# Optimization experiments

Hardware: AMD Instinct MI355X
Metric: run time of the kernel (lower is better)

Reference implementation:

```python
import jax, jax.numpy as jnp
import numpy as np

N = 4_194_304
NUM_ITER = 6
DAMPING = 0.95
TOL = 1e-06
EPS = 1e-12


def _translate_x(dx):
    """4x4 homogeneous translation along the optical (x) axis."""
    return jnp.eye(4, dtype=dx.dtype).at[0, 3].set(dx)


def setup_inputs() -> dict:
    key = jax.random.key(0)
    k1, k2, k3 = jax.random.split(key, 3)
    # Ray origins: near x = -10, transverse spread within/around the aperture
    px = -10.0 + 0.5 * jax.random.normal(k1, (N, 1), dtype=jnp.float32)
    pyz = 8.0 * jax.random.normal(k2, (N, 2), dtype=jnp.float32)
    P = jnp.concatenate([px, pyz], axis=-1)
    # Ray directions: mostly +x, small transverse components, normalized
    vyz = 0.05 * jax.random.normal(k3, (N, 2), dtype=jnp.float32)
    V = jnp.concatenate([jnp.ones((N, 1), jnp.float32), vyz], axis=-1)
    V = V / jnp.linalg.norm(V, axis=-1, keepdims=True)
    tf = jnp.eye(4, dtype=jnp.float32)
    return {
        "P": P,
        "V": V,
        "tf": tf,
        "diameter": jnp.float32(50.0),
        "C": jnp.float32(0.02),
        "anchors": jnp.zeros((2,), jnp.float32),
        "scale": jnp.float32(1.0),
        "normalize": jnp.asarray(False),
    }


def reference(P, V, tf, diameter, C, anchors, scale, normalize):
    # normalize: curvature interpreted relative to semi-diameter
    C_eff = jnp.where(normalize, C * 2.0 / diameter, C)
    s2 = scale * scale

    def sag(r2):  # scaled spherical sag: f = scale * g(r2/scale^2)
        u = r2 / s2
        root = jnp.sqrt(jnp.clip(1.0 - C_eff * C_eff * u, EPS))
        return scale * C_eff * u / (1.0 + root)

    def sag_grad(y, z):  # (df/dy, df/dz) = C*(y,z) / (scale*sqrt(1-C^2 u))
        u = (y * y + z * z) / s2
        root = jnp.sqrt(jnp.clip(1.0 - C_eff * C_eff * u, EPS))
        k = C_eff / (scale * root)
        return k * y, k * z

    # anchors shift the surface along x by fractions of the edge sag (extent)
    extent = sag(jnp.square(diameter * 0.5))
    surface_tf = tf @ _translate_x(-anchors[0] * extent)
    next_tf = tf @ _translate_x((anchors[1] - anchors[0]) * extent)

    # Rays into surface-local frame
    R = surface_tf[:3, :3]
    tv = surface_tf[:3, 3]
    Pl = (P - tv) @ R  # [N,3] = R^T (P - t)
    Vl = V @ R
    vx, vy, vz = Vl[:, 0], Vl[:, 1], Vl[:, 2]

    safe_vx = jnp.where(jnp.abs(vx) > EPS, vx, EPS)
    t = -Pl[:, 0] / safe_vx  # init: intersection with plane x=0

    # Damped Newton on F(t) = sag(y(t),z(t)) - x(t)
    for _ in range(NUM_ITER):
        p = Pl + t[:, None] * Vl
        y, z = p[:, 1], p[:, 2]
        F = sag(y * y + z * z) - p[:, 0]
        gy, gz = sag_grad(y, z)
        dF = gy * vy + gz * vz - vx
        dF = jnp.where(jnp.abs(dF) > EPS, dF, EPS)
        t = t - DAMPING * F / dF

    p = Pl + t[:, None] * Vl
    y, z = p[:, 1], p[:, 2]
    r2 = y * y + z * z
    F = sag(r2) - p[:, 0]
    gy, gz = sag_grad(y, z)
    # implicit-surface normal: grad(sag(y,z) - x) = (-1, gy, gz), normalized
    n_local = jnp.stack([-jnp.ones_like(gy), gy, gz], axis=-1)
    n_local = n_local / jnp.linalg.norm(n_local, axis=-1, keepdims=True)
    normals = n_local @ R.T  # back to global frame

    valid = (r2 <= jnp.square(diameter * 0.5)) & (jnp.abs(F) < 100.0 * TOL)
    return t, normals, valid, surface_tf, next_tf
```

## Files before the change

kernel.cpp:

```cpp
#include <hip/hip_runtime.h>

#define F_EPS 1e-12f
#define F_DAMPING 0.95f
#define N_ITER 6

struct Params {
    float R[9];
    float tv[3];
    float C_eff;
    float s2;
    float scale;
    float half_d2;
    float inv_s2;
};

__global__ void setup_kernel(const float* __restrict__ tf,
                             const float* __restrict__ diameter,
                             const float* __restrict__ C,
                             const float* __restrict__ anchors,
                             const float* __restrict__ scale,
                             const unsigned char* __restrict__ normalize,
                             float* __restrict__ out_tail,
                             Params* __restrict__ params)
{
#pragma clang fp contract(off)
    if (threadIdx.x != 0 || blockIdx.x != 0) return;
    float d  = diameter[0];
    float c  = C[0];
    float sc = scale[0];
    bool  nrm = (normalize[0] != 0);
    float C_eff = nrm ? (c * 2.0f / d) : c;
    float s2 = sc * sc;
    float hr = d * 0.5f;
    float hr2 = hr * hr;
    float u = hr2 / s2;
    float root = sqrtf(fmaxf(1.0f - (C_eff * C_eff) * u, F_EPS));
    float extent = sc * C_eff * u / (1.0f + root);
    float a0 = anchors[0], a1 = anchors[1];
    float dx0 = -a0 * extent;
    float dx1 = (a1 - a0) * extent;
    for (int i = 0; i < 4; ++i) {
        for (int j = 0; j < 4; ++j) {
            float v = tf[i * 4 + j];
            float sv = (j == 3) ? (tf[i * 4 + 0] * dx0 + v) : v;
            float nv = (j == 3) ? (tf[i * 4 + 0] * dx1 + v) : v;
            out_tail[i * 4 + j]      = sv;
            out_tail[16 + i * 4 + j] = nv;
        }
    }
    for (int k = 0; k < 3; ++k) {
        for (int j = 0; j < 3; ++j)
            params->R[k * 3 + j] = tf[k * 4 + j];
        params->tv[k] = tf[k * 4 + 0] * dx0 + tf[k * 4 + 3];
    }
    params->C_eff   = C_eff;
    params->s2      = s2;
    params->scale   = sc;
    params->half_d2 = hr2;
    params->inv_s2  = 1.0f / s2;
}

__launch_bounds__(256)
__global__ void trace_kernel(const float* __restrict__ P,
                             const float* __restrict__ V,
                             const Params* __restrict__ pp,
                             float* __restrict__ out,
                             int n)
{
#pragma clang fp contract(off)
    int tid = blockIdx.x * blockDim.x + threadIdx.x;
    int base = tid * 4;
    if (base >= n) return;

    float R0 = pp->R[0], R1 = pp->R[1], R2 = pp->R[2];
    float R3 = pp->R[3], R4 = pp->R[4], R5 = pp->R[5];
    float R6 = pp->R[6], R7 = pp->R[7], R8 = pp->R[8];
    float tv0 = pp->tv[0], tv1 = pp->tv[1], tv2 = pp->tv[2];
    float C_eff = pp->C_eff, s2 = pp->s2, scale = pp->scale, half_d2 = pp->half_d2;
    float inv_s2 = pp->inv_s2;
    float ce2 = C_eff * C_eff;
    float sC  = scale * C_eff;
    float a_num = sC * inv_s2;
    float ce2s  = ce2 * inv_s2;
    float Cs    = C_eff / scale;

    float Px[4], Py[4], Pz[4], Vx[4], Vy[4], Vz[4];
    if (base + 4 <= n) {
        const float4* P4 = reinterpret_cast<const float4*>(P + (size_t)base * 3);
        const float4* V4 = reinterpret_cast<const float4*>(V + (size_t)base * 3);
        float4 pa = P4[0], pb = P4[1], pc = P4[2];
        float4 va = V4[0], vb = V4[1], vc = V4[2];
        Px[0] = pa.x; Py[0] = pa.y; Pz[0] = pa.z;
        Px[1] = pa.w; Py[1] = pb.x; Pz[1] = pb.y;
        Px[2] = pb.z; Py[2] = pb.w; Pz[2] = pc.x;
        Px[3] = pc.y; Py[3] = pc.z; Pz[3] = pc.w;
        Vx[0] = va.x; Vy[0] = va.y; Vz[0] = va.z;
        Vx[1] = va.w; Vy[1] = vb.x; Vz[1] = vb.y;
        Vx[2] = vb.z; Vy[2] = vb.w; Vz[2] = vc.x;
        Vx[3] = vc.y; Vy[3] = vc.z; Vz[3] = vc.w;
    } else {
        for (int r = 0; r < 4; ++r) {
            int i = base + r;
            if (i < n) {
                Px[r] = P[(size_t)i * 3 + 0]; Py[r] = P[(size_t)i * 3 + 1]; Pz[r] = P[(size_t)i * 3 + 2];
                Vx[r] = V[(size_t)i * 3 + 0]; Vy[r] = V[(size_t)i * 3 + 1]; Vz[r] = V[(size_t)i * 3 + 2];
            } else {
                Px[r] = 0.0f; Py[r] = 0.0f; Pz[r] = 0.0f;
                Vx[r] = 1.0f; Vy[r] = 0.0f; Vz[r] = 0.0f;
            }
        }
    }

    float tres[4], nxo[4], nyo[4], nzo[4], val[4];
#pragma unroll
    for (int r = 0; r < 4; ++r) {
        float px0 = Px[r] - tv0, py0 = Py[r] - tv1, pz0 = Pz[r] - tv2;
        float Plx = px0 * R0 + py0 * R3 + pz0 * R6;
        float Ply = px0 * R1 + py0 * R4 + pz0 * R7;
        float Plz = px0 * R2 + py0 * R5 + pz0 * R8;
        float vx = Vx[r] * R0 + Vy[r] * R3 + Vz[r] * R6;
        float vy = Vx[r] * R1 + Vy[r] * R4 + Vz[r] * R7;
        float vz = Vx[r] * R2 + Vy[r] * R5 + Vz[r] * R8;
        float safe_vx = (fabsf(vx) > F_EPS) ? vx : F_EPS;
        float t = (-Plx) / safe_vx;

#pragma unroll
        for (int it = 0; it < N_ITER; ++it) {
            float pxx = fmaf(t, vx, Plx);
            float py  = fmaf(t, vy, Ply);
            float pz  = fmaf(t, vz, Plz);
            float r2  = fmaf(py, py, pz * pz);
            float m   = fmaxf(fmaf(-ce2s, r2, 1.0f), F_EPS);
            float rsq = __builtin_amdgcn_rsqf(m);
            float root = m * rsq;
            float k    = Cs * rsq;
            float ird  = __builtin_amdgcn_rcpf(1.0f + root);
            float F    = fmaf(a_num * r2, ird, -pxx);
            float gy = k * py, gz = k * pz;
            float dF = fmaf(gy, vy, fmaf(gz, vz, -vx));
            dF = (fabsf(dF) > F_EPS) ? dF : F_EPS;
            float idF = __builtin_amdgcn_rcpf(dF);
            t = fmaf(-F_DAMPING * F, idF, t);
        }

        float pxx = Plx + t * vx;
        float py  = Ply + t * vy;
        float pz  = Plz + t * vz;
        float r2  = py * py + pz * pz;
        float u   = r2 / s2;
        float root = sqrtf(fmaxf(1.0f - ce2 * u, F_EPS));
        float F = sC * u / (1.0f + root) - pxx;
        float k = C_eff / (scale * root);
        float gy = k * py, gz = k * pz;
        float nn = sqrtf(1.0f + gy * gy + gz * gz);
        float nlx = (-1.0f) / nn, nly = gy / nn, nlz = gz / nn;
        nxo[r] = nlx * R0 + nly * R1 + nlz * R2;
        nyo[r] = nlx * R3 + nly * R4 + nlz * R5;
        nzo[r] = nlx * R6 + nly * R7 + nlz * R8;
        tres[r] = t;
        val[r]  = ((r2 <= half_d2) && (fabsf(F) < 1e-4f)) ? 1.0f : 0.0f;
    }

    float* t_out = out;
    float* n_out = out + (size_t)n;
    float* v_out = out + (size_t)n * 4;
    if (base + 4 <= n) {
        *reinterpret_cast<float4*>(t_out + base) = make_float4(tres[0], tres[1], tres[2], tres[3]);
        float4* N4 = reinterpret_cast<float4*>(n_out + (size_t)base * 3);
        N4[0] = make_float4(nxo[0], nyo[0], nzo[0], nxo[1]);
        N4[1] = make_float4(nyo[1], nzo[1], nxo[2], nyo[2]);
        N4[2] = make_float4(nzo[2], nxo[3], nyo[3], nzo[3]);
        *reinterpret_cast<float4*>(v_out + base) = make_float4(val[0], val[1], val[2], val[3]);
    } else {
        for (int r = 0; r < 4; ++r) {
            int i = base + r;
            if (i < n) {
                t_out[i] = tres[r];
                n_out[(size_t)i * 3 + 0] = nxo[r];
                n_out[(size_t)i * 3 + 1] = nyo[r];
                n_out[(size_t)i * 3 + 2] = nzo[r];
                v_out[i] = val[r];
            }
        }
    }
}

extern "C" void kernel_launch(void* const* d_in, const int* in_sizes, int n_in,
                              void* d_out, int out_size, void* d_ws, size_t ws_size,
                              hipStream_t stream) {
    const float* P  = (const float*)d_in[0];
    const float* V  = (const float*)d_in[1];
    const float* tf = (const float*)d_in[2];
    const float* diameter = (const float*)d_in[3];
    const float* C  = (const float*)d_in[4];
    const float* anchors = (const float*)d_in[5];
    const float* scale = (const float*)d_in[6];
    const unsigned char* normalize = (const unsigned char*)d_in[7];
    int n = in_sizes[0] / 3;
    float* out = (float*)d_out;
    float* out_tail = out + (size_t)n * 5;
    Params* params = (Params*)d_ws;

    setup_kernel<<<1, 1, 0, stream>>>(tf, diameter, C, anchors, scale, normalize,
                                      out_tail, params);
    int threads = 256;
    int nthreads = (n + 3) / 4;
    int blocks = (nthreads + threads - 1) / threads;
    trace_kernel<<<blocks, threads, 0, stream>>>(P, V, params, out, n);
}
```

Before: 182.6 us.

## Interleave Newton iterations across four rays and use fast approximate math

Restructures the per-thread loop so each Newton iteration is applied to all four rays before moving to the next, which gives the scheduler four independent dependency chains to overlap. Also removes the fp-contract-off pragma so FMAs can fuse, and replaces the exact divisions and sqrt in the init and final normal/validity computation with hardware rcp/rsq intrinsics. This trades exact IEEE division/sqrt for approximate results, which can slightly change t, the normals and the validity threshold decisions.

```diff
diff --git a/kernel.cpp b/kernel.cpp
--- a/kernel.cpp
+++ b/kernel.cpp
@@ -67,7 +67,6 @@
                              float* __restrict__ out,
                              int n)
 {
-#pragma clang fp contract(off)
     int tid = blockIdx.x * blockDim.x + threadIdx.x;
     int base = tid * 4;
     if (base >= n) return;
@@ -76,7 +75,7 @@
     float R3 = pp->R[3], R4 = pp->R[4], R5 = pp->R[5];
     float R6 = pp->R[6], R7 = pp->R[7], R8 = pp->R[8];
     float tv0 = pp->tv[0], tv1 = pp->tv[1], tv2 = pp->tv[2];
-    float C_eff = pp->C_eff, s2 = pp->s2, scale = pp->scale, half_d2 = pp->half_d2;
+    float C_eff = pp->C_eff, scale = pp->scale, half_d2 = pp->half_d2;
     float inv_s2 = pp->inv_s2;
     float ce2 = C_eff * C_eff;
     float sC  = scale * C_eff;
@@ -111,24 +110,27 @@
         }
     }
 
-    float tres[4], nxo[4], nyo[4], nzo[4], val[4];
+    float Plx[4], Ply[4], Plz[4], vx[4], vy[4], vz[4], t[4];
 #pragma unroll
     for (int r = 0; r < 4; ++r) {
         float px0 = Px[r] - tv0, py0 = Py[r] - tv1, pz0 = Pz[r] - tv2;
-        float Plx = px0 * R0 + py0 * R3 + pz0 * R6;
-        float Ply = px0 * R1 + py0 * R4 + pz0 * R7;
-        float Plz = px0 * R2 + py0 * R5 + pz0 * R8;
-        float vx = Vx[r] * R0 + Vy[r] * R3 + Vz[r] * R6;
-        float vy = Vx[r] * R1 + Vy[r] * R4 + Vz[r] * R7;
-        float vz = Vx[r] * R2 + Vy[r] * R5 + Vz[r] * R8;
-        float safe_vx = (fabsf(vx) > F_EPS) ? vx : F_EPS;
-        float t = (-Plx) / safe_vx;
-
-#pragma unroll
-        for (int it = 0; it < N_ITER; ++it) {
-            float pxx = fmaf(t, vx, Plx);
-            float py  = fmaf(t, vy, Ply);
-            float pz  = fmaf(t, vz, Plz);
+        Plx[r] = px0 * R0 + py0 * R3 + pz0 * R6;
+        Ply[r] = px0 * R1 + py0 * R4 + pz0 * R7;
+        Plz[r] = px0 * R2 + py0 * R5 + pz0 * R8;
+        vx[r] = Vx[r] * R0 + Vy[r] * R3 + Vz[r] * R6;
+        vy[r] = Vx[r] * R1 + Vy[r] * R4 + Vz[r] * R7;
+        vz[r] = Vx[r] * R2 + Vy[r] * R5 + Vz[r] * R8;
+        float safe_vx = (fabsf(vx[r]) > F_EPS) ? vx[r] : F_EPS;
+        t[r] = (-Plx[r]) * __builtin_amdgcn_rcpf(safe_vx);
+    }
+
+#pragma unroll
+    for (int it = 0; it < N_ITER; ++it) {
+#pragma unroll
+        for (int r = 0; r < 4; ++r) {
+            float pxx = fmaf(t[r], vx[r], Plx[r]);
+            float py  = fmaf(t[r], vy[r], Ply[r]);
+            float pz  = fmaf(t[r], vz[r], Plz[r]);
             float r2  = fmaf(py, py, pz * pz);
             float m   = fmaxf(fmaf(-ce2s, r2, 1.0f), F_EPS);
             float rsq = __builtin_amdgcn_rsqf(m);
@@ -136,28 +138,33 @@
             float k    = Cs * rsq;
             float ird  = __builtin_amdgcn_rcpf(1.0f + root);
             float F    = fmaf(a_num * r2, ird, -pxx);
-            float gy = k * py, gz = k * pz;
-            float dF = fmaf(gy, vy, fmaf(gz, vz, -vx));
+            float dF = fmaf(k * py, vy[r], fmaf(k * pz, vz[r], -vx[r]));
             dF = (fabsf(dF) > F_EPS) ? dF : F_EPS;
-            float idF = __builtin_amdgcn_rcpf(dF);
-            t = fmaf(-F_DAMPING * F, idF, t);
-        }
-
-        float pxx = Plx + t * vx;
-        float py  = Ply + t * vy;
-        float pz  = Plz + t * vz;
-        float r2  = py * py + pz * pz;
-        float u   = r2 / s2;
-        float root = sqrtf(fmaxf(1.0f - ce2 * u, F_EPS));
-        float F = sC * u / (1.0f + root) - pxx;
-        float k = C_eff / (scale * root);
+            t[r] = fmaf(-F_DAMPING * F, __builtin_amdgcn_rcpf(dF), t[r]);
+        }
+    }
+
+    float tres[4], nxo[4], nyo[4], nzo[4], val[4];
+#pragma unroll
+    for (int r = 0; r < 4; ++r) {
+        float pxx = fmaf(t[r], vx[r], Plx[r]);
+        float py  = fmaf(t[r], vy[r], Ply[r]);
+        float pz  = fmaf(t[r], vz[r], Plz[r]);
+        float r2  = fmaf(py, py, pz * pz);
+        float m   = fmaxf(fmaf(-ce2s, r2, 1.0f), F_EPS);
+        float rsq = __builtin_amdgcn_rsqf(m);
+        float root = m * rsq;
+        float k    = Cs * rsq;
+        float ird  = __builtin_amdgcn_rcpf(1.0f + root);
+        float F    = fmaf(a_num * r2, ird, -pxx);
         float gy = k * py, gz = k * pz;
-        float nn = sqrtf(1.0f + gy * gy + gz * gz);
-        float nlx = (-1.0f) / nn, nly = gy / nn, nlz = gz / nn;
+        float nn2 = fmaf(gy, gy, fmaf(gz, gz, 1.0f));
+        float irn = __builtin_amdgcn_rsqf(nn2);
+        float nlx = -irn, nly = gy * irn, nlz = gz * irn;
         nxo[r] = nlx * R0 + nly * R1 + nlz * R2;
         nyo[r] = nlx * R3 + nly * R4 + nlz * R5;
         nzo[r] = nlx * R6 + nly * R7 + nlz * R8;
-        tres[r] = t;
+        tres[r] = t[r];
         val[r]  = ((r2 <= half_d2) && (fabsf(F) < 1e-4f)) ? 1.0f : 0.0f;
     }
 
```

New measurement: 180.5 us. Within noise of the previous version (-1.1%).
